# Performance work log

Measured on AMD Instinct MI355X. Metric: run time of the kernel, lower is better.

Reference implementation:

```python
import jax, jax.numpy as jnp
import numpy as np
from jax import lax

H = 256  # hidden_size


def _conv1d(x, w, b):
    # x: (N, Cin, L), w: (Cout, Cin, K) -> (N, Cout, L-K+1), VALID, stride 1
    y = lax.conv_general_dilated(x, w, window_strides=(1,), padding='VALID',
                                 dimension_numbers=('NCH', 'OIH', 'NCH'))
    return y + b[None, :, None]


def _gru_dir(x, Wih, Whh, bih, bhh):
    # x: (L, N, H). Torch GRU cell equations.
    L, N, _ = x.shape
    gi = jnp.einsum('lnh,gh->lng', x, Wih) + bih  # (L, N, 3H) precomputed input gates
    h0 = jnp.zeros((N, H), x.dtype)

    def step(h, gi_t):
        gh = h @ Whh.T + bhh                       # (N, 3H)
        ir, iz, inn = jnp.split(gi_t, 3, axis=-1)
        hr, hz, hn = jnp.split(gh, 3, axis=-1)
        r = jax.nn.sigmoid(ir + hr)
        z = jax.nn.sigmoid(iz + hz)
        n = jnp.tanh(inn + r * hn)
        h_new = (1.0 - z) * n + z * h
        return h_new, h_new

    hT, ys = lax.scan(step, h0, gi)
    return ys, hT  # (L, N, H), (N, H)


def setup_inputs() -> dict:
    key = jax.random.key(0)
    ks = jax.random.split(key, 14)
    N, C, L = 32, 13, 4096
    s = 0.1
    inp = {
        'X': jax.random.normal(ks[0], (N, C, L), jnp.float32),
        'W1': jax.random.normal(ks[1], (H // 2, C, 3), jnp.float32) * s,
        'b1': jax.random.normal(ks[2], (H // 2,), jnp.float32) * s,
        'W2': jax.random.normal(ks[3], (H, H // 2, 3), jnp.float32) * s,
        'b2': jax.random.normal(ks[4], (H,), jnp.float32) * s,
        'Wih_f': jax.random.normal(ks[5], (3 * H, H), jnp.float32) * s,
        'Whh_f': jax.random.normal(ks[6], (3 * H, H), jnp.float32) * s,
        'bih_f': jax.random.normal(ks[7], (3 * H,), jnp.float32) * s,
        'bhh_f': jax.random.normal(ks[8], (3 * H,), jnp.float32) * s,
        'Wih_b': jax.random.normal(ks[9], (3 * H, H), jnp.float32) * s,
        'Whh_b': jax.random.normal(ks[10], (3 * H, H), jnp.float32) * s,
        'bih_b': jax.random.normal(ks[11], (3 * H,), jnp.float32) * s,
        'bhh_b': jax.random.normal(ks[12], (3 * H,), jnp.float32) * s,
    }
    return inp


def reference(X, W1, b1, W2, b2, Wih_f, Whh_f, bih_f, bhh_f,
              Wih_b, Whh_b, bih_b, bhh_b):
    # dropouts are identity in eval mode; N>1 so squeeze() is a no-op
    x = _conv1d(X, W1, b1)           # (N, H/2, L-2)
    x = _conv1d(x, W2, b2)           # (N, H,   L-4)
    x = x[:, :, ::2]                 # MaxPool1d(kernel=1, stride=2) == stride-2 subsample
    x = jnp.transpose(x, (2, 0, 1))  # (L', N, H)

    out_f, hT_f = _gru_dir(x, Wih_f, Whh_f, bih_f, bhh_f)
    # backward direction: reverse time, scan, reverse outputs
    out_b_rev, hT_b = _gru_dir(x[::-1], Wih_b, Whh_b, bih_b, bhh_b)
    out_b = out_b_rev[::-1]

    # original: fwd + flip(bwd along FEATURE axis), averaged, ReLU (faithful to np.flip(axis=-1))
    comb = jax.nn.relu((out_f + out_b[:, :, ::-1]) * 0.5)  # (L', N, H)
    hidden_last = hT_b[None]                                # hidden[-1].unsqueeze(0): (1, N, H)
    return comb, hidden_last
```

## Files before the change

kernel.cpp:

```cpp
#include <hip/hip_runtime.h>
#include <hip/hip_fp16.h>
#include <cstdint>
#include <cstddef>

#define L_SEQ 2046
#define NBATCH 32
#define HID 256
#define M_PAD 65536

typedef _Float16 h2vec  __attribute__((ext_vector_type(2)));
typedef _Float16 half8v __attribute__((ext_vector_type(8)));
typedef float    f32x4  __attribute__((ext_vector_type(4)));

static __device__ __forceinline__ uint32_t pack2(float a, float b) {
  __half2 h = __floats2half2_rn(a, b);
  return __builtin_bit_cast(uint32_t, h);
}

static __device__ __forceinline__ float fdot2u(uint32_t w, uint32_t h, float c) {
#if __has_builtin(__builtin_amdgcn_fdot2)
  return __builtin_amdgcn_fdot2(__builtin_bit_cast(h2vec, w),
                                __builtin_bit_cast(h2vec, h), c, false);
#else
  __half2 a = __builtin_bit_cast(__half2, w);
  __half2 b = __builtin_bit_cast(__half2, h);
  float2 fa = __half22float2(a), fb = __half22float2(b);
  return c + fa.x * fb.x + fa.y * fb.y;
#endif
}

static __device__ __forceinline__ void gload_lds16(const void* g, void* l) {
  __builtin_amdgcn_global_load_lds(
      (const __attribute__((address_space(1))) void*)g,
      (__attribute__((address_space(3))) void*)l, 16, 0, 0);
}

__global__ void k_conv_im2col(const float* __restrict__ X,
                              const float* __restrict__ W1,
                              const float* __restrict__ b1,
                              __half* __restrict__ A1h) {
  int j   = threadIdx.x;
  int row = blockIdx.x;
  int l2 = row >> 5, n = row & 31;
  float v = 0.f;
  if (l2 < L_SEQ) {
    int ci = j / 3;
    int k  = j - 3 * ci;
    int p  = 2 * l2 + k;
    const float* xb = X + (size_t)n * 13 * 4096 + p;
    const float* w  = W1 + ci * 39;
    float acc = b1[ci];
#pragma unroll
    for (int c = 0; c < 13; c++) {
      const float* xp = xb + (size_t)c * 4096;
      acc += xp[0] * w[3*c+0] + xp[1] * w[3*c+1] + xp[2] * w[3*c+2];
    }
    v = acc;
  }
  A1h[(size_t)row * 384 + j] = __float2half(v);
}

__global__ void k_cvt_h(const float* __restrict__ src, __half* __restrict__ dst,
                        int nelem) {
  int i = blockIdx.x * 256 + threadIdx.x;
  if (i < nelem) dst[i] = __float2half(src[i]);
}

__global__ __launch_bounds__(256, 3) void k_gemm_mfma(
    const __half* __restrict__ A, const __half* __restrict__ Bh,
    const float* __restrict__ bias, __half* __restrict__ C,
    int K, int ldC, int col_off) {
  __shared__ __half Asl[128 * 64];
  __shared__ __half Bsl[128 * 64];
  const int tid  = threadIdx.x;
  const int wave = tid >> 6, lane = tid & 63;
  const int m_blk = blockIdx.x * 128;
  const int n_blk = blockIdx.y * 128;
  const int wm = wave >> 1, wn = wave & 1;

  f32x4 acc[4][4];
#pragma unroll
  for (int i = 0; i < 4; i++)
#pragma unroll
    for (int j = 0; j < 4; j++) acc[i][j] = (f32x4)0.f;

  int srow[4], sko[4];
#pragma unroll
  for (int i = 0; i < 4; i++) {
    int s = (i * 4 + wave) * 64 + lane;
    srow[i] = s >> 3;
    sko[i]  = (s & 7) ^ ((s >> 3) & 7);
  }

  for (int kc = 0; kc < K; kc += 64) {
#pragma unroll
    for (int i = 0; i < 4; i++) {
      int s = (i * 4 + wave) * 64 + lane;
      gload_lds16(A + (size_t)(m_blk + srow[i]) * K + kc + sko[i] * 8,
                  &Asl[s * 8]);
    }
#pragma unroll
    for (int i = 0; i < 4; i++) {
      int s = (i * 4 + wave) * 64 + lane;
      gload_lds16(Bh + (size_t)(n_blk + srow[i]) * K + kc + sko[i] * 8,
                  &Bsl[s * 8]);
    }
    __syncthreads();
#pragma unroll
    for (int kb = 0; kb < 2; kb++) {
      half8v af[4], bf[4];
#pragma unroll
      for (int mi = 0; mi < 4; mi++) {
        int row = wm * 64 + mi * 16 + (lane & 15);
        int c   = (kb * 4 + (lane >> 4)) ^ (row & 7);
        af[mi] = *(const half8v*)&Asl[row * 64 + c * 8];
      }
#pragma unroll
      for (int ni = 0; ni < 4; ni++) {
        int row = wn * 64 + ni * 16 + (lane & 15);
        int c   = (kb * 4 + (lane >> 4)) ^ (row & 7);
        bf[ni] = *(const half8v*)&Bsl[row * 64 + c * 8];
      }
#pragma unroll
      for (int mi = 0; mi < 4; mi++)
#pragma unroll
        for (int ni = 0; ni < 4; ni++)
          acc[mi][ni] = __builtin_amdgcn_mfma_f32_16x16x32_f16(
              af[mi], bf[ni], acc[mi][ni], 0, 0, 0);
    }
    __syncthreads();
  }
#pragma unroll
  for (int ni = 0; ni < 4; ni++) {
    int col = wn * 64 + ni * 16 + (lane & 15);
    float bj = bias[n_blk + col];
#pragma unroll
    for (int mi = 0; mi < 4; mi++) {
      int row0 = m_blk + wm * 64 + mi * 16 + (lane >> 4) * 4;
#pragma unroll
      for (int r = 0; r < 4; r++) {
        C[(size_t)(row0 + r) * ldC + col_off + n_blk + col] =
            __float2half(acc[mi][ni][r] + bj);
      }
    }
  }
}

__global__ void k_packw(const float* __restrict__ Whh_f,
                        const float* __restrict__ Whh_b,
                        uint4* __restrict__ Wpk) {
  int idx = blockIdx.x * 256 + threadIdx.x;
  int d   = idx / 24576;
  int r   = idx - d * 24576;
  int jq  = r >> 9;
  int tid = r & 511;
  int q   = jq / 3, gt = jq - 3 * q;
  int lane = tid & 63, wave = tid >> 6;
  int kh = lane & 1, g = wave * 32 + (lane >> 1);
  const float* W = d ? Whh_b : Whh_f;
  const float* src = W + (size_t)(gt * 256 + g) * 256 + kh * 128 + 8 * q;
  uint4 o;
  o.x = pack2(src[0], src[1]);
  o.y = pack2(src[2], src[3]);
  o.z = pack2(src[4], src[5]);
  o.w = pack2(src[6], src[7]);
  Wpk[(size_t)idx] = o;
}

__global__ __attribute__((amdgpu_flat_work_group_size(512, 512),
                          amdgpu_waves_per_eu(2, 2)))
void k_gru(
    const __half* __restrict__ gih, const uint4* __restrict__ Wpk,
    const float* __restrict__ bhh_f, const float* __restrict__ bhh_b,
    float* __restrict__ outF, __half* __restrict__ outBh,
    float* __restrict__ hT) {
  const int blk = blockIdx.x;
  const int dir = blk >> 5;
  const int n   = blk & 31;
  const int tid = threadIdx.x;
  const int lane = tid & 63;
  const int kh  = lane & 1;
  const int g   = (tid >> 6) * 32 + (lane >> 1);

  const float* bhh = dir ? bhh_b : bhh_f;

  uint4 wv[48];
  {
    const uint4* wp = Wpk + (size_t)dir * 24576 + tid;
#pragma unroll
    for (int j = 0; j < 48; j++) wv[j] = wp[j * 512];
#pragma unroll
    for (int j = 0; j < 48; j++) {
      asm volatile("" : "+v"(wv[j].x), "+v"(wv[j].y), "+v"(wv[j].z), "+v"(wv[j].w));
    }
  }
  const float bh0 = bhh[g];
  const float bh1 = bhh[256 + g];
  const float bh2 = bhh[512 + g];

  __shared__ __align__(16) __half hs[2][256];
  if (tid < 128) ((uint32_t*)hs)[tid] = 0u;
  float hp = 0.f;

  const __half* gr = gih + ((size_t)(dir ? (size_t)(L_SEQ - 1) * NBATCH : 0) + n) * 1536
                         + dir * 768 + g;
  const ptrdiff_t gstep = dir ? -(ptrdiff_t)(NBATCH * 1536) : (ptrdiff_t)(NBATCH * 1536);
  __half pi0 = __float2half(0.f), pi1 = pi0, pi2 = pi0;
  if (kh == 0) { pi0 = gr[0]; pi1 = gr[256]; pi2 = gr[512]; }
  __syncthreads();

  for (int t = 0; t < L_SEQ; t++) {
    const uint4* hb = (const uint4*)hs[t & 1];
    float a0 = 0.f, a1 = 0.f, a2 = 0.f;
#pragma unroll
    for (int q = 0; q < 16; q++) {
      uint4 hq = hb[q * 2 + kh];
      uint4 u0 = wv[q * 3 + 0];
      uint4 u1 = wv[q * 3 + 1];
      uint4 u2 = wv[q * 3 + 2];
      a0 = fdot2u(u0.x, hq.x, a0);
      a0 = fdot2u(u0.y, hq.y, a0);
      a0 = fdot2u(u0.z, hq.z, a0);
      a0 = fdot2u(u0.w, hq.w, a0);
      a1 = fdot2u(u1.x, hq.x, a1);
      a1 = fdot2u(u1.y, hq.y, a1);
      a1 = fdot2u(u1.z, hq.z, a1);
      a1 = fdot2u(u1.w, hq.w, a1);
      a2 = fdot2u(u2.x, hq.x, a2);
      a2 = fdot2u(u2.y, hq.y, a2);
      a2 = fdot2u(u2.z, hq.z, a2);
      a2 = fdot2u(u2.w, hq.w, a2);
    }
    a0 += __shfl_xor(a0, 1);
    a1 += __shfl_xor(a1, 1);
    a2 += __shfl_xor(a2, 1);

    if (kh == 0) {
      float hr = a0 + bh0;
      float hz = a1 + bh1;
      float hn = a2 + bh2;
      float ir  = __half2float(pi0);
      float iz  = __half2float(pi1);
      float inn = __half2float(pi2);
      float rr = 1.f / (1.f + __expf(-(ir + hr)));
      float zz = 1.f / (1.f + __expf(-(iz + hz)));
      float e  = __expf(2.f * (inn + rr * hn));
      float nn = 1.f - 2.f / (e + 1.f);
      float hnew = (1.f - zz) * nn + zz * hp;
      hp = hnew;
      __half hh = __float2half(hnew);
      int swi = ((g & 127) >> 3) * 16 + (g >> 7) * 8 + (g & 7);
      hs[(t + 1) & 1][swi] = hh;
      const int l = dir ? (L_SEQ - 1 - t) : t;
      uint32_t oi = ((uint32_t)l * NBATCH + n) * HID + g;
      if (dir == 0) outF[oi] = hnew;
      else          outBh[oi] = hh;
      gr += gstep;
      if (t + 1 < L_SEQ) { pi0 = gr[0]; pi1 = gr[256]; pi2 = gr[512]; }
    }
    __syncthreads();
  }
  if (dir == 1 && kh == 0) hT[n * HID + g] = hp;
}

__global__ void k_combine(float* __restrict__ outF,
                          const __half* __restrict__ outBh) {
  int idx = blockIdx.x * 256 + threadIdx.x;
  int c = idx & 255;
  float v = 0.5f * (outF[idx] + __half2float(outBh[idx + 255 - 2 * c]));
  outF[idx] = v > 0.f ? v : 0.f;
}

extern "C" void kernel_launch(void* const* d_in, const int* in_sizes, int n_in,
                              void* d_out, int out_size, void* d_ws, size_t ws_size,
                              hipStream_t stream) {
  const float* X     = (const float*)d_in[0];
  const float* W1    = (const float*)d_in[1];
  const float* b1    = (const float*)d_in[2];
  const float* W2    = (const float*)d_in[3];
  const float* b2    = (const float*)d_in[4];
  const float* Wih_f = (const float*)d_in[5];
  const float* Whh_f = (const float*)d_in[6];
  const float* bih_f = (const float*)d_in[7];
  const float* bhh_f = (const float*)d_in[8];
  const float* Wih_b = (const float*)d_in[9];
  const float* Whh_b = (const float*)d_in[10];
  const float* bih_b = (const float*)d_in[11];
  const float* bhh_b = (const float*)d_in[12];

  char* wsb = (char*)d_ws;
  __half* gih   = (__half*)(wsb);
  __half* W2h   = (__half*)(wsb);
  __half* A1h   = (__half*)(wsb + 201326592);
  __half* outBh = (__half*)(wsb + 201326592);
  uint4*  Wpk   = (uint4*)(wsb + 234848768);
  __half* WihfH = (__half*)(wsb + 235635200);
  __half* WihbH = (__half*)(wsb + 236028416);

  float*  outF  = (float*)d_out;
  __half* xsubh = (__half*)d_out;
  float*  hT    = outF + (size_t)L_SEQ * NBATCH * HID;

  k_conv_im2col<<<dim3(M_PAD), 384, 0, stream>>>(X, W1, b1, A1h);
  k_cvt_h<<<dim3(384), 256, 0, stream>>>(W2, W2h, 98304);
  k_gemm_mfma<<<dim3(512, 2), 256, 0, stream>>>(A1h, W2h, b2, xsubh, 384, 256, 0);
  k_cvt_h<<<dim3(768), 256, 0, stream>>>(Wih_f, WihfH, 196608);
  k_cvt_h<<<dim3(768), 256, 0, stream>>>(Wih_b, WihbH, 196608);
  k_packw<<<dim3(192), 256, 0, stream>>>(Whh_f, Whh_b, Wpk);
  k_gemm_mfma<<<dim3(512, 6), 256, 0, stream>>>(xsubh, WihfH, bih_f, gih, 256, 1536, 0);
  k_gemm_mfma<<<dim3(512, 6), 256, 0, stream>>>(xsubh, WihbH, bih_b, gih, 256, 1536, 768);
  k_gru<<<dim3(64), 512, 0, stream>>>(gih, Wpk, bhh_f, bhh_b, outF, outBh, hT);
  k_combine<<<dim3(65472), 256, 0, stream>>>(outF, outBh);
}
```

Baseline: 3.053 ms.

## Restructure GRU recurrence to one thread per gate row with LDS gate exchange

The recurrent GRU kernel goes from 512 threads, each computing half-dot-products for three gates and combining them with a lane shuffle, to 768 threads, each owning one full row of Whh. Weights are repacked so every thread holds its whole 256-wide row in registers, 32 uint4 instead of 48. Gate pre-activations are exchanged through shared memory, and only one wave in three computes the activations. This shortens each thread's dependent dot-product chain and spreads the work over more waves, at the cost of an extra __syncthreads per timestep, idle activation waves, and broadcast LDS reads of h.

```diff
diff --git a/kernel.cpp b/kernel.cpp
--- a/kernel.cpp
+++ b/kernel.cpp
@@ -146,19 +146,16 @@
   }
 }
 
-__global__ void k_packw(const float* __restrict__ Whh_f,
-                        const float* __restrict__ Whh_b,
-                        uint4* __restrict__ Wpk) {
+__global__ void k_packw2(const float* __restrict__ Whh_f,
+                         const float* __restrict__ Whh_b,
+                         uint4* __restrict__ Wpk) {
   int idx = blockIdx.x * 256 + threadIdx.x;
   int d   = idx / 24576;
   int r   = idx - d * 24576;
-  int jq  = r >> 9;
-  int tid = r & 511;
-  int q   = jq / 3, gt = jq - 3 * q;
-  int lane = tid & 63, wave = tid >> 6;
-  int kh = lane & 1, g = wave * 32 + (lane >> 1);
+  int w   = r / 768;
+  int j   = r - w * 768;
   const float* W = d ? Whh_b : Whh_f;
-  const float* src = W + (size_t)(gt * 256 + g) * 256 + kh * 128 + 8 * q;
+  const float* src = W + (size_t)j * 256 + w * 8;
   uint4 o;
   o.x = pack2(src[0], src[1]);
   o.y = pack2(src[2], src[3]);
@@ -167,8 +164,8 @@
   Wpk[(size_t)idx] = o;
 }
 
-__global__ __attribute__((amdgpu_flat_work_group_size(512, 512),
-                          amdgpu_waves_per_eu(2, 2)))
+__global__ __attribute__((amdgpu_flat_work_group_size(768, 768),
+                          amdgpu_waves_per_eu(3, 3)))
 void k_gru(
     const __half* __restrict__ gih, const uint4* __restrict__ Wpk,
     const float* __restrict__ bhh_f, const float* __restrict__ bhh_b,
@@ -178,20 +175,21 @@
   const int dir = blk >> 5;
   const int n   = blk & 31;
   const int tid = threadIdx.x;
+  const int wv_ = tid >> 6;
   const int lane = tid & 63;
-  const int kh  = lane & 1;
-  const int g   = (tid >> 6) * 32 + (lane >> 1);
+  const bool is_act = (wv_ % 3) == 0;
+  const int g = (wv_ / 3) * 64 + lane;
 
   const float* bhh = dir ? bhh_b : bhh_f;
 
-  uint4 wv[48];
+  uint4 wv[32];
   {
     const uint4* wp = Wpk + (size_t)dir * 24576 + tid;
 #pragma unroll
-    for (int j = 0; j < 48; j++) wv[j] = wp[j * 512];
-#pragma unroll
-    for (int j = 0; j < 48; j++) {
-      asm volatile("" : "+v"(wv[j].x), "+v"(wv[j].y), "+v"(wv[j].z), "+v"(wv[j].w));
+    for (int w = 0; w < 32; w++) wv[w] = wp[w * 768];
+#pragma unroll
+    for (int w = 0; w < 32; w++) {
+      asm volatile("" : "+v"(wv[w].x), "+v"(wv[w].y), "+v"(wv[w].z), "+v"(wv[w].w));
     }
   }
   const float bh0 = bhh[g];
@@ -199,6 +197,7 @@
   const float bh2 = bhh[512 + g];
 
   __shared__ __align__(16) __half hs[2][256];
+  __shared__ float a_lds[768];
   if (tid < 128) ((uint32_t*)hs)[tid] = 0u;
   float hp = 0.f;
 
@@ -206,39 +205,28 @@
                          + dir * 768 + g;
   const ptrdiff_t gstep = dir ? -(ptrdiff_t)(NBATCH * 1536) : (ptrdiff_t)(NBATCH * 1536);
   __half pi0 = __float2half(0.f), pi1 = pi0, pi2 = pi0;
-  if (kh == 0) { pi0 = gr[0]; pi1 = gr[256]; pi2 = gr[512]; }
+  if (is_act) { pi0 = gr[0]; pi1 = gr[256]; pi2 = gr[512]; }
   __syncthreads();
 
   for (int t = 0; t < L_SEQ; t++) {
     const uint4* hb = (const uint4*)hs[t & 1];
-    float a0 = 0.f, a1 = 0.f, a2 = 0.f;
-#pragma unroll
-    for (int q = 0; q < 16; q++) {
-      uint4 hq = hb[q * 2 + kh];
-      uint4 u0 = wv[q * 3 + 0];
-      uint4 u1 = wv[q * 3 + 1];
-      uint4 u2 = wv[q * 3 + 2];
-      a0 = fdot2u(u0.x, hq.x, a0);
-      a0 = fdot2u(u0.y, hq.y, a0);
-      a0 = fdot2u(u0.z, hq.z, a0);
-      a0 = fdot2u(u0.w, hq.w, a0);
-      a1 = fdot2u(u1.x, hq.x, a1);
-      a1 = fdot2u(u1.y, hq.y, a1);
-      a1 = fdot2u(u1.z, hq.z, a1);
-      a1 = fdot2u(u1.w, hq.w, a1);
-      a2 = fdot2u(u2.x, hq.x, a2);
-      a2 = fdot2u(u2.y, hq.y, a2);
-      a2 = fdot2u(u2.z, hq.z, a2);
-      a2 = fdot2u(u2.w, hq.w, a2);
-    }
-    a0 += __shfl_xor(a0, 1);
-    a1 += __shfl_xor(a1, 1);
-    a2 += __shfl_xor(a2, 1);
-
-    if (kh == 0) {
-      float hr = a0 + bh0;
-      float hz = a1 + bh1;
-      float hn = a2 + bh2;
+    float a = 0.f;
+#pragma unroll
+    for (int w = 0; w < 32; w++) {
+      uint4 hq = hb[w];
+      uint4 u  = wv[w];
+      a = fdot2u(u.x, hq.x, a);
+      a = fdot2u(u.y, hq.y, a);
+      a = fdot2u(u.z, hq.z, a);
+      a = fdot2u(u.w, hq.w, a);
+    }
+    a_lds[tid] = a;
+    __syncthreads();
+
+    if (is_act) {
+      float hr = a_lds[g]       + bh0;
+      float hz = a_lds[256 + g] + bh1;
+      float hn = a_lds[512 + g] + bh2;
       float ir  = __half2float(pi0);
       float iz  = __half2float(pi1);
       float inn = __half2float(pi2);
@@ -249,8 +237,7 @@
       float hnew = (1.f - zz) * nn + zz * hp;
       hp = hnew;
       __half hh = __float2half(hnew);
-      int swi = ((g & 127) >> 3) * 16 + (g >> 7) * 8 + (g & 7);
-      hs[(t + 1) & 1][swi] = hh;
+      hs[(t + 1) & 1][g] = hh;
       const int l = dir ? (L_SEQ - 1 - t) : t;
       uint32_t oi = ((uint32_t)l * NBATCH + n) * HID + g;
       if (dir == 0) outF[oi] = hnew;
@@ -260,7 +247,7 @@
     }
     __syncthreads();
   }
-  if (dir == 1 && kh == 0) hT[n * HID + g] = hp;
+  if (dir == 1 && is_act) hT[n * HID + g] = hp;
 }
 
 __global__ void k_combine(float* __restrict__ outF,
@@ -306,9 +293,9 @@
   k_gemm_mfma<<<dim3(512, 2), 256, 0, stream>>>(A1h, W2h, b2, xsubh, 384, 256, 0);
   k_cvt_h<<<dim3(768), 256, 0, stream>>>(Wih_f, WihfH, 196608);
   k_cvt_h<<<dim3(768), 256, 0, stream>>>(Wih_b, WihbH, 196608);
-  k_packw<<<dim3(192), 256, 0, stream>>>(Whh_f, Whh_b, Wpk);
+  k_packw2<<<dim3(192), 256, 0, stream>>>(Whh_f, Whh_b, Wpk);
   k_gemm_mfma<<<dim3(512, 6), 256, 0, stream>>>(xsubh, WihfH, bih_f, gih, 256, 1536, 0);
   k_gemm_mfma<<<dim3(512, 6), 256, 0, stream>>>(xsubh, WihbH, bih_b, gih, 256, 1536, 768);
-  k_gru<<<dim3(64), 512, 0, stream>>>(gih, Wpk, bhh_f, bhh_b, outF, outBh, hT);
+  k_gru<<<dim3(64), 768, 0, stream>>>(gih, Wpk, bhh_f, bhh_b, outF, outBh, hT);
   k_combine<<<dim3(65472), 256, 0, stream>>>(outF, outBh);
 }
```

Result: slower. 3.125 ms (+2.4%).

## Split GRU recurrence between MFMA waves and fdot2 waves, stage gates in LDS

Applied to the files above, without the earlier changes.

The recurrent GRU kernel now splits its work by wave. Four waves compute half of the hidden units with 16x16x32 f16 MFMA instructions using a newly packed weight layout. The other four waves keep the fdot2 path for the other half, and both groups share h through two LDS layouts. Input gate rows are prefetched into LDS with global_load_lds double buffering, and the r/z recurrent biases are folded into the input-projection GEMM bias. This aims to shorten the per-timestep latency of the serial recurrence, at the cost of more LDS traffic and a heterogeneous wave schedule that must balance across the barrier.

```diff
diff --git a/kernel.cpp b/kernel.cpp
--- a/kernel.cpp
+++ b/kernel.cpp
@@ -11,10 +11,15 @@
 typedef _Float16 h2vec  __attribute__((ext_vector_type(2)));
 typedef _Float16 half8v __attribute__((ext_vector_type(8)));
 typedef float    f32x4  __attribute__((ext_vector_type(4)));
+typedef unsigned short u16x4 __attribute__((ext_vector_type(4)));
 
 static __device__ __forceinline__ uint32_t pack2(float a, float b) {
   __half2 h = __floats2half2_rn(a, b);
   return __builtin_bit_cast(uint32_t, h);
+}
+
+static __device__ __forceinline__ float u16f(unsigned short u) {
+  return __half2float(__builtin_bit_cast(__half, u));
 }
 
 static __device__ __forceinline__ float fdot2u(uint32_t w, uint32_t h, float c) {
@@ -66,6 +71,20 @@
   if (i < nelem) dst[i] = __float2half(src[i]);
 }
 
+__global__ void k_biascomb(const float* __restrict__ bih_f,
+                           const float* __restrict__ bhh_f,
+                           const float* __restrict__ bih_b,
+                           const float* __restrict__ bhh_b,
+                           float* __restrict__ outFb, float* __restrict__ outBb) {
+  int i = blockIdx.x * 256 + threadIdx.x;
+  if (i < 768) {
+    float af = i < 512 ? bhh_f[i] : 0.f;
+    float ab = i < 512 ? bhh_b[i] : 0.f;
+    outFb[i] = bih_f[i] + af;
+    outBb[i] = bih_b[i] + ab;
+  }
+}
+
 __global__ __launch_bounds__(256, 3) void k_gemm_mfma(
     const __half* __restrict__ A, const __half* __restrict__ Bh,
     const float* __restrict__ bias, __half* __restrict__ C,
@@ -146,17 +165,17 @@
   }
 }
 
-__global__ void k_packw(const float* __restrict__ Whh_f,
-                        const float* __restrict__ Whh_b,
-                        uint4* __restrict__ Wpk) {
+__global__ void k_packw_v(const float* __restrict__ Whh_f,
+                          const float* __restrict__ Whh_b,
+                          uint4* __restrict__ Wv) {
   int idx = blockIdx.x * 256 + threadIdx.x;
-  int d   = idx / 24576;
-  int r   = idx - d * 24576;
-  int jq  = r >> 9;
-  int tid = r & 511;
-  int q   = jq / 3, gt = jq - 3 * q;
-  int lane = tid & 63, wave = tid >> 6;
-  int kh = lane & 1, g = wave * 32 + (lane >> 1);
+  int d    = idx / 12288;
+  int r    = idx - d * 12288;
+  int jq   = r >> 8;
+  int cons = r & 255;
+  int q  = jq / 3, gt = jq - 3 * q;
+  int vw = cons >> 6, lane = cons & 63;
+  int kh = lane & 1, g = 128 + vw * 32 + (lane >> 1);
   const float* W = d ? Whh_b : Whh_f;
   const float* src = W + (size_t)(gt * 256 + g) * 256 + kh * 128 + 8 * q;
   uint4 o;
@@ -164,13 +183,38 @@
   o.y = pack2(src[2], src[3]);
   o.z = pack2(src[4], src[5]);
   o.w = pack2(src[6], src[7]);
-  Wpk[(size_t)idx] = o;
+  Wv[(size_t)idx] = o;
+}
+
+__global__ void k_packw_m(const float* __restrict__ Whh_f,
+                          const float* __restrict__ Whh_b,
+                          uint4* __restrict__ Wm) {
+  int idx = blockIdx.x * 256 + threadIdx.x;
+  int d  = idx / 12288;
+  int r  = idx - d * 12288;
+  int mw = r / 3072;
+  int r2 = r - mw * 3072;
+  int f  = r2 >> 6;
+  int l  = r2 & 63;
+  int t6 = f >> 3, ks = f & 7;
+  int gate = t6 >> 1, j = t6 & 1;
+  int row = gate * 256 + mw * 32 + j * 16 + (l & 15);
+  int k0  = ks * 32 + (l >> 4) * 8;
+  const float* W = d ? Whh_b : Whh_f;
+  const float* src = W + (size_t)row * 256 + k0;
+  uint4 o;
+  o.x = pack2(src[0], src[1]);
+  o.y = pack2(src[2], src[3]);
+  o.z = pack2(src[4], src[5]);
+  o.w = pack2(src[6], src[7]);
+  Wm[(size_t)idx] = o;
 }
 
 __global__ __attribute__((amdgpu_flat_work_group_size(512, 512),
                           amdgpu_waves_per_eu(2, 2)))
 void k_gru(
-    const __half* __restrict__ gih, const uint4* __restrict__ Wpk,
+    const __half* __restrict__ gih,
+    const uint4* __restrict__ Wv, const uint4* __restrict__ Wm,
     const float* __restrict__ bhh_f, const float* __restrict__ bhh_b,
     float* __restrict__ outF, __half* __restrict__ outBh,
     float* __restrict__ hT) {
@@ -178,89 +222,200 @@
   const int dir = blk >> 5;
   const int n   = blk & 31;
   const int tid = threadIdx.x;
+  const int wave = tid >> 6;
   const int lane = tid & 63;
-  const int kh  = lane & 1;
-  const int g   = (tid >> 6) * 32 + (lane >> 1);
-
   const float* bhh = dir ? bhh_b : bhh_f;
 
-  uint4 wv[48];
-  {
-    const uint4* wp = Wpk + (size_t)dir * 24576 + tid;
-#pragma unroll
-    for (int j = 0; j < 48; j++) wv[j] = wp[j * 512];
-#pragma unroll
-    for (int j = 0; j < 48; j++) {
-      asm volatile("" : "+v"(wv[j].x), "+v"(wv[j].y), "+v"(wv[j].z), "+v"(wv[j].w));
-    }
-  }
-  const float bh0 = bhh[g];
-  const float bh1 = bhh[256 + g];
-  const float bh2 = bhh[512 + g];
-
-  __shared__ __align__(16) __half hs[2][256];
-  if (tid < 128) ((uint32_t*)hs)[tid] = 0u;
-  float hp = 0.f;
-
-  const __half* gr = gih + ((size_t)(dir ? (size_t)(L_SEQ - 1) * NBATCH : 0) + n) * 1536
-                         + dir * 768 + g;
-  const ptrdiff_t gstep = dir ? -(ptrdiff_t)(NBATCH * 1536) : (ptrdiff_t)(NBATCH * 1536);
-  __half pi0 = __float2half(0.f), pi1 = pi0, pi2 = pi0;
-  if (kh == 0) { pi0 = gr[0]; pi1 = gr[256]; pi2 = gr[512]; }
-  __syncthreads();
-
-  for (int t = 0; t < L_SEQ; t++) {
-    const uint4* hb = (const uint4*)hs[t & 1];
-    float a0 = 0.f, a1 = 0.f, a2 = 0.f;
-#pragma unroll
-    for (int q = 0; q < 16; q++) {
-      uint4 hq = hb[q * 2 + kh];
-      uint4 u0 = wv[q * 3 + 0];
-      uint4 u1 = wv[q * 3 + 1];
-      uint4 u2 = wv[q * 3 + 2];
-      a0 = fdot2u(u0.x, hq.x, a0);
-      a0 = fdot2u(u0.y, hq.y, a0);
-      a0 = fdot2u(u0.z, hq.z, a0);
-      a0 = fdot2u(u0.w, hq.w, a0);
-      a1 = fdot2u(u1.x, hq.x, a1);
-      a1 = fdot2u(u1.y, hq.y, a1);
-      a1 = fdot2u(u1.z, hq.z, a1);
-      a1 = fdot2u(u1.w, hq.w, a1);
-      a2 = fdot2u(u2.x, hq.x, a2);
-      a2 = fdot2u(u2.y, hq.y, a2);
-      a2 = fdot2u(u2.z, hq.z, a2);
-      a2 = fdot2u(u2.w, hq.w, a2);
-    }
-    a0 += __shfl_xor(a0, 1);
-    a1 += __shfl_xor(a1, 1);
-    a2 += __shfl_xor(a2, 1);
-
-    if (kh == 0) {
-      float hr = a0 + bh0;
-      float hz = a1 + bh1;
-      float hn = a2 + bh2;
-      float ir  = __half2float(pi0);
-      float iz  = __half2float(pi1);
-      float inn = __half2float(pi2);
-      float rr = 1.f / (1.f + __expf(-(ir + hr)));
-      float zz = 1.f / (1.f + __expf(-(iz + hz)));
-      float e  = __expf(2.f * (inn + rr * hn));
-      float nn = 1.f - 2.f / (e + 1.f);
-      float hnew = (1.f - zz) * nn + zz * hp;
-      hp = hnew;
-      __half hh = __float2half(hnew);
-      int swi = ((g & 127) >> 3) * 16 + (g >> 7) * 8 + (g & 7);
-      hs[(t + 1) & 1][swi] = hh;
-      const int l = dir ? (L_SEQ - 1 - t) : t;
-      uint32_t oi = ((uint32_t)l * NBATCH + n) * HID + g;
-      if (dir == 0) outF[oi] = hnew;
-      else          outBh[oi] = hh;
-      gr += gstep;
-      if (t + 1 < L_SEQ) { pi0 = gr[0]; pi1 = gr[256]; pi2 = gr[512]; }
-    }
+  __shared__ __align__(16) __half h_pl[2][256];
+  __shared__ __align__(16) __half h_sw[2][256];
+  __shared__ __align__(16) __half gi_lds[2][768];
+
+  if (tid < 128) {
+    ((uint32_t*)h_pl)[tid] = 0u;
+    ((uint32_t*)h_sw)[tid] = 0u;
+  }
+
+  const __half* gsrc0 = gih +
+      ((size_t)(dir ? (size_t)(L_SEQ - 1) * NBATCH : 0) + n) * 1536 + dir * 768;
+  const ptrdiff_t gstepB = (dir ? -(ptrdiff_t)(NBATCH * 1536)
+                               :  (ptrdiff_t)(NBATCH * 1536)) * 2;
+
+  if (wave < 4) {
+    const int mw  = wave;
+    const int hi4 = lane >> 4;
+    const bool al = (lane & 15) == 0;
+
+    uint4 wm[48];
+    {
+      const uint4* wp = Wm + ((size_t)(dir * 4 + mw) * 48) * 64 + lane;
+#pragma unroll
+      for (int f = 0; f < 48; f++) wm[f] = wp[f * 64];
+    }
+    f32x4 bhn[2];
+    bhn[0] = *(const f32x4*)&bhh[512 + mw * 32 + 0 * 16 + hi4 * 4];
+    bhn[1] = *(const f32x4*)&bhh[512 + mw * 32 + 1 * 16 + hi4 * 4];
+    f32x4 hp[2];
+    hp[0] = (f32x4)0.f; hp[1] = (f32x4)0.f;
+
+    const char* gcur = (const char*)gsrc0;
+    if (mw == 0) {
+      gload_lds16(gcur + lane * 16, (char*)&gi_lds[0][0] + lane * 16);
+      if (lane < 32)
+        gload_lds16(gcur + 1024 + lane * 16, (char*)&gi_lds[0][0] + 1024 + lane * 16);
+    }
+    gcur += gstepB;
     __syncthreads();
-  }
-  if (dir == 1 && kh == 0) hT[n * HID + g] = hp;
+
+    int cur = 0;
+    for (int t = 0; t < L_SEQ; t++) {
+      if (mw == 0 && t + 1 < L_SEQ) {
+        gload_lds16(gcur + lane * 16, (char*)&gi_lds[cur ^ 1][0] + lane * 16);
+        if (lane < 32)
+          gload_lds16(gcur + 1024 + lane * 16,
+                      (char*)&gi_lds[cur ^ 1][0] + 1024 + lane * 16);
+      }
+      gcur += gstepB;
+
+      f32x4 acc[6];
+#pragma unroll
+      for (int i = 0; i < 6; i++) acc[i] = (f32x4)0.f;
+      {
+        const __half* hb = h_pl[cur];
+#pragma unroll
+        for (int ks = 0; ks < 8; ks++) {
+          half8v bf = *(const half8v*)&hb[ks * 32 + hi4 * 8];
+#pragma unroll
+          for (int t6 = 0; t6 < 6; t6++)
+            acc[t6] = __builtin_amdgcn_mfma_f32_16x16x32_f16(
+                __builtin_bit_cast(half8v, wm[t6 * 8 + ks]), bf, acc[t6], 0, 0, 0);
+        }
+      }
+
+      if (al) {
+        const int lidx = dir ? (L_SEQ - 1 - t) : t;
+        const __half* gi = gi_lds[cur];
+#pragma unroll
+        for (int j = 0; j < 2; j++) {
+          const int g0 = mw * 32 + j * 16 + hi4 * 4;
+          u16x4 vr = *(const u16x4*)&gi[g0];
+          u16x4 vz = *(const u16x4*)&gi[256 + g0];
+          u16x4 vn = *(const u16x4*)&gi[512 + g0];
+          float hnew[4];
+#pragma unroll
+          for (int rr = 0; rr < 4; rr++) {
+            float hr = acc[j][rr];
+            float hz = acc[2 + j][rr];
+            float hn = acc[4 + j][rr] + bhn[j][rr];
+            float ir  = u16f(vr[rr]);
+            float iz  = u16f(vz[rr]);
+            float inn = u16f(vn[rr]);
+            float rv = 1.f / (1.f + __expf(-(ir + hr)));
+            float zz = 1.f / (1.f + __expf(-(iz + hz)));
+            float e  = __expf(2.f * (inn + rv * hn));
+            float nn = 1.f - 2.f / (e + 1.f);
+            hnew[rr] = (1.f - zz) * nn + zz * hp[j][rr];
+            hp[j][rr] = hnew[rr];
+          }
+          uint2 pk;
+          pk.x = pack2(hnew[0], hnew[1]);
+          pk.y = pack2(hnew[2], hnew[3]);
+          *(uint2*)&h_pl[cur ^ 1][g0] = pk;
+          const int sli = ((g0 >> 3) * 2) * 8 + (g0 & 7);
+          *(uint2*)&h_sw[cur ^ 1][sli] = pk;
+          const size_t oi = ((size_t)lidx * NBATCH + n) * HID + g0;
+          if (dir == 0) {
+            f32x4 o; o[0] = hnew[0]; o[1] = hnew[1]; o[2] = hnew[2]; o[3] = hnew[3];
+            *(f32x4*)&outF[oi] = o;
+          } else {
+            *(uint2*)&outBh[oi] = pk;
+          }
+        }
+      }
+      __syncthreads();
+      cur ^= 1;
+    }
+    if (dir == 1 && al) {
+#pragma unroll
+      for (int j = 0; j < 2; j++) {
+        const int g0 = mw * 32 + j * 16 + hi4 * 4;
+        f32x4 o; o[0] = hp[j][0]; o[1] = hp[j][1]; o[2] = hp[j][2]; o[3] = hp[j][3];
+        *(f32x4*)&hT[(size_t)n * HID + g0] = o;
+      }
+    }
+  } else {
+    const int vw = wave - 4;
+    const int kh = lane & 1;
+    const int g  = 128 + vw * 32 + (lane >> 1);
+
+    uint4 wv[48];
+    {
+      const uint4* wp = Wv + (size_t)dir * 12288 + vw * 64 + lane;
+#pragma unroll
+      for (int jq = 0; jq < 48; jq++) wv[jq] = wp[jq * 256];
+#pragma unroll
+      for (int jq = 0; jq < 48; jq++) {
+        asm volatile("" : "+v"(wv[jq].x), "+v"(wv[jq].y), "+v"(wv[jq].z), "+v"(wv[jq].w));
+      }
+    }
+    const float bh2 = bhh[512 + g];
+    float hp = 0.f;
+    __syncthreads();
+
+    int cur = 0;
+    for (int t = 0; t < L_SEQ; t++) {
+      const uint4* hb = (const uint4*)h_sw[cur];
+      float a0 = 0.f, a1 = 0.f, a2 = 0.f;
+#pragma unroll
+      for (int q = 0; q < 16; q++) {
+        uint4 hq = hb[q * 2 + kh];
+        uint4 u0 = wv[q * 3 + 0];
+        uint4 u1 = wv[q * 3 + 1];
+        uint4 u2 = wv[q * 3 + 2];
+        a0 = fdot2u(u0.x, hq.x, a0);
+        a0 = fdot2u(u0.y, hq.y, a0);
+        a0 = fdot2u(u0.z, hq.z, a0);
+        a0 = fdot2u(u0.w, hq.w, a0);
+        a1 = fdot2u(u1.x, hq.x, a1);
+        a1 = fdot2u(u1.y, hq.y, a1);
+        a1 = fdot2u(u1.z, hq.z, a1);
+        a1 = fdot2u(u1.w, hq.w, a1);
+        a2 = fdot2u(u2.x, hq.x, a2);
+        a2 = fdot2u(u2.y, hq.y, a2);
+        a2 = fdot2u(u2.z, hq.z, a2);
+        a2 = fdot2u(u2.w, hq.w, a2);
+      }
+      a0 += __shfl_xor(a0, 1);
+      a1 += __shfl_xor(a1, 1);
+      a2 += __shfl_xor(a2, 1);
+
+      if (kh == 0) {
+        const __half* gi = gi_lds[cur];
+        float ir  = __half2float(gi[g]);
+        float iz  = __half2float(gi[256 + g]);
+        float inn = __half2float(gi[512 + g]);
+        float hr = a0;
+        float hz = a1;
+        float hn = a2 + bh2;
+        float rv = 1.f / (1.f + __expf(-(ir + hr)));
+        float zz = 1.f / (1.f + __expf(-(iz + hz)));
+        float e  = __expf(2.f * (inn + rv * hn));
+        float nn = 1.f - 2.f / (e + 1.f);
+        float hnew = (1.f - zz) * nn + zz * hp;
+        hp = hnew;
+        __half hh = __float2half(hnew);
+        const int swi = ((g & 127) >> 3) * 16 + (g >> 7) * 8 + (g & 7);
+        h_sw[cur ^ 1][swi] = hh;
+        h_pl[cur ^ 1][g]   = hh;
+        const int lidx = dir ? (L_SEQ - 1 - t) : t;
+        const uint32_t oi = ((uint32_t)lidx * NBATCH + n) * HID + g;
+        if (dir == 0) outF[oi] = hnew;
+        else          outBh[oi] = hh;
+      }
+      __syncthreads();
+      cur ^= 1;
+    }
+    if (dir == 1 && kh == 0) hT[n * HID + g] = hp;
+  }
 }
 
 __global__ void k_combine(float* __restrict__ outF,
@@ -293,9 +448,12 @@
   __half* W2h   = (__half*)(wsb);
   __half* A1h   = (__half*)(wsb + 201326592);
   __half* outBh = (__half*)(wsb + 201326592);
-  uint4*  Wpk   = (uint4*)(wsb + 234848768);
+  uint4*  Wv    = (uint4*)(wsb + 234848768);
+  uint4*  Wm    = (uint4*)(wsb + 235241984);
   __half* WihfH = (__half*)(wsb + 235635200);
   __half* WihbH = (__half*)(wsb + 236028416);
+  float*  biasF = (float*)(wsb + 236421632);
+  float*  biasB = (float*)(wsb + 236424704);
 
   float*  outF  = (float*)d_out;
   __half* xsubh = (__half*)d_out;
@@ -306,9 +464,11 @@
   k_gemm_mfma<<<dim3(512, 2), 256, 0, stream>>>(A1h, W2h, b2, xsubh, 384, 256, 0);
   k_cvt_h<<<dim3(768), 256, 0, stream>>>(Wih_f, WihfH, 196608);
   k_cvt_h<<<dim3(768), 256, 0, stream>>>(Wih_b, WihbH, 196608);
-  k_packw<<<dim3(192), 256, 0, stream>>>(Whh_f, Whh_b, Wpk);
-  k_gemm_mfma<<<dim3(512, 6), 256, 0, stream>>>(xsubh, WihfH, bih_f, gih, 256, 1536, 0);
-  k_gemm_mfma<<<dim3(512, 6), 256, 0, stream>>>(xsubh, WihbH, bih_b, gih, 256, 1536, 768);
-  k_gru<<<dim3(64), 512, 0, stream>>>(gih, Wpk, bhh_f, bhh_b, outF, outBh, hT);
+  k_packw_v<<<dim3(96), 256, 0, stream>>>(Whh_f, Whh_b, Wv);
+  k_packw_m<<<dim3(96), 256, 0, stream>>>(Whh_f, Whh_b, Wm);
+  k_biascomb<<<dim3(3), 256, 0, stream>>>(bih_f, bhh_f, bih_b, bhh_b, biasF, biasB);
+  k_gemm_mfma<<<dim3(512, 6), 256, 0, stream>>>(xsubh, WihfH, biasF, gih, 256, 1536, 0);
+  k_gemm_mfma<<<dim3(512, 6), 256, 0, stream>>>(xsubh, WihbH, biasB, gih, 256, 1536, 768);
+  k_gru<<<dim3(64), 512, 0, stream>>>(gih, Wv, Wm, bhh_f, bhh_b, outF, outBh, hT);
   k_combine<<<dim3(65472), 256, 0, stream>>>(outF, outBh);
 }
```

Measured after the change: 4.404 ms. 1.44x slower.
